# Kernel tuning notes

Measured on AMD Instinct MI355X. Metric: run time of the kernel, lower is better.

## Reference

```python
import jax, jax.numpy as jnp
from jax import lax
import numpy as np

B, C, L = 64, 32, 1549
HID = 256          # LSTM hidden per direction
NH, DK = 8, 64     # n_heads, d_k ; NH*DK = 2*HID = 512
D2 = 2 * HID


def setup_inputs() -> dict:
    key = jax.random.key(0)
    ks = jax.random.split(key, 32)
    r = lambda i, shape: jax.random.normal(ks[i], shape, jnp.float32) * 0.05
    inp = {"x": jax.random.normal(ks[0], (B, C, L), jnp.float32)}
    inp["conv_w"] = r(1, (C, C, 16))
    inp["conv_b"] = r(2, (C,))
    inp["bn_gamma"] = 1.0 + r(3, (C,))
    inp["bn_beta"] = r(4, (C,))
    inp["bn_mean"] = r(5, (C,))
    inp["bn_var"] = jax.random.uniform(ks[6], (C,), jnp.float32, 0.5, 1.5)
    names = [("W_ih0f", (4*HID, C)), ("W_hh0f", (4*HID, HID)), ("b0f", (4*HID,)),
             ("W_ih0b", (4*HID, C)), ("W_hh0b", (4*HID, HID)), ("b0b", (4*HID,)),
             ("W_ih1f", (4*HID, D2)), ("W_hh1f", (4*HID, HID)), ("b1f", (4*HID,)),
             ("W_ih1b", (4*HID, D2)), ("W_hh1b", (4*HID, HID)), ("b1b", (4*HID,)),
             ("Wq", (D2, D2)), ("bq", (D2,)), ("Wk", (D2, D2)), ("bk", (D2,)),
             ("Wv", (D2, D2)), ("bv", (D2,)), ("ln_g", (D2,)), ("ln_b", (D2,)),
             ("fc_w", (1, D2)), ("fc_b", (1,))]
    for j, (n, s) in enumerate(names):
        inp[n] = r(7 + j, s)
    inp["ln_g"] = 1.0 + inp["ln_g"]
    return inp


def _lstm_dir(xg, W_hh, reverse):
    # xg: [B,S,4H] precomputed input-to-gate projections (+biases); PyTorch gate order i,f,g,o
    if reverse:
        xg = xg[:, ::-1]
    Bq = xg.shape[0]
    H = W_hh.shape[1]
    def step(carry, g_t):
        h, c = carry
        g = g_t + h @ W_hh.T
        i, f, gg, o = jnp.split(g, 4, axis=-1)
        c = jax.nn.sigmoid(f) * c + jax.nn.sigmoid(i) * jnp.tanh(gg)
        h = jax.nn.sigmoid(o) * jnp.tanh(c)
        return (h, c), h
    init = (jnp.zeros((Bq, H), xg.dtype), jnp.zeros((Bq, H), xg.dtype))
    _, hs = lax.scan(step, init, jnp.swapaxes(xg, 0, 1))
    hs = jnp.swapaxes(hs, 0, 1)
    return hs[:, ::-1] if reverse else hs


def _bilstm(x, Wif, Whf, bf, Wib, Whb, bb):
    hf = _lstm_dir(jnp.einsum('bsd,gd->bsg', x, Wif) + bf, Whf, False)
    hb = _lstm_dir(jnp.einsum('bsd,gd->bsg', x, Wib) + bb, Whb, True)
    return jnp.concatenate([hf, hb], axis=-1)


def _forward(x, conv_w, conv_b, bn_gamma, bn_beta, bn_mean, bn_var,
             W_ih0f, W_hh0f, b0f, W_ih0b, W_hh0b, b0b,
             W_ih1f, W_hh1f, b1f, W_ih1b, W_hh1b, b1b,
             Wq, bq, Wk, bk, Wv, bv, ln_g, ln_b, fc_w, fc_b):
    # conv1d (k=16, pad=1) + BatchNorm (eval) + relu + maxpool(k=3, stride=3)
    h = lax.conv_general_dilated(x, conv_w, (1,), [(1, 1)],
                                 dimension_numbers=('NCH', 'OIH', 'NCH')) + conv_b[None, :, None]
    h = (h - bn_mean[None, :, None]) * jax.lax.rsqrt(bn_var[None, :, None] + 1e-5) \
        * bn_gamma[None, :, None] + bn_beta[None, :, None]
    h = jax.nn.relu(h)
    h = lax.reduce_window(h, -jnp.inf, lax.max, (1, 1, 3), (1, 1, 3), 'VALID')
    h = jnp.transpose(h, (0, 2, 1))            # [B, S, C]
    # 2-layer bidirectional LSTM (eval: inter-layer dropout inactive)
    out = _bilstm(h, W_ih0f, W_hh0f, b0f, W_ih0b, W_hh0b, b0b)
    out = _bilstm(out, W_ih1f, W_hh1f, b1f, W_ih1b, W_hh1b, b1b)   # [B, S, 512]
    Bq, S, _ = out.shape
    q = (out @ Wq.T + bq).reshape(Bq, S, NH, DK).transpose(0, 2, 1, 3)
    k = (out @ Wk.T + bk).reshape(Bq, S, NH, DK).transpose(0, 2, 1, 3)
    v = (out @ Wv.T + bv).reshape(Bq, S, NH, DK).transpose(0, 2, 1, 3)
    attn = jnp.einsum('bhsd,bhtd->bhst', q, k) / np.sqrt(DK)
    # NOTE: original uses nn.LogSoftmax(dim=1) -> log-softmax over the HEAD axis
    la = jax.nn.log_softmax(attn, axis=1)
    ctx = jnp.einsum('bhst,bhtd->bhsd', la, v)
    ctx = jnp.transpose(ctx, (0, 2, 1, 3)).reshape(Bq, S, D2)
    r = out + ctx
    mu = jnp.mean(r, axis=-1, keepdims=True)
    var = jnp.mean((r - mu) ** 2, axis=-1, keepdims=True)
    r = (r - mu) * jax.lax.rsqrt(var + 1e-5) * ln_g + ln_b
    pooled = jnp.mean(r, axis=1)               # len_reduction='mean'
    return pooled @ fc_w.T + fc_b              # [B, 1]


def reference(x, conv_w, conv_b, bn_gamma, bn_beta, bn_mean, bn_var,
              W_ih0f, W_hh0f, b0f, W_ih0b, W_hh0b, b0b,
              W_ih1f, W_hh1f, b1f, W_ih1b, W_hh1b, b1b,
              Wq, bq, Wk, bk, Wv, bv, ln_g, ln_b, fc_w, fc_b):
    return _forward(x, conv_w, conv_b, bn_gamma, bn_beta, bn_mean, bn_var,
                    W_ih0f, W_hh0f, b0f, W_ih0b, W_hh0b, b0b,
                    W_ih1f, W_hh1f, b1f, W_ih1b, W_hh1b, b1b,
                    Wq, bq, Wk, bk, Wv, bv, ln_g, ln_b, fc_w, fc_b)
```

## Files before the change

### kernel.cpp

```cpp
#include <hip/hip_runtime.h>
#include <hip/hip_bf16.h>
#include <math.h>

#define L_IN 1549
#define S_OUT 512

typedef __hip_bfloat16 bf16;
typedef __attribute__((ext_vector_type(8))) short bfrag;
typedef __attribute__((ext_vector_type(4))) float f32x4;

__device__ __forceinline__ float bfbits2f(unsigned short u) {
    union { unsigned int i; float f; } x;
    x.i = ((unsigned int)u) << 16;
    return x.f;
}
__device__ __forceinline__ unsigned short f2bfbits(float f) {
    union { float f; unsigned int i; } x; x.f = f;
    unsigned int lsb = (x.i >> 16) & 1;
    return (unsigned short)((x.i + 0x7fff + lsb) >> 16);
}
__device__ __forceinline__ float4 cv8(const float* p) {
    float4 u0 = *(const float4*)p;
    float4 u1 = *(const float4*)(p + 4);
    union { float4 f; unsigned short h[8]; } o;
    o.h[0] = f2bfbits(u0.x); o.h[1] = f2bfbits(u0.y);
    o.h[2] = f2bfbits(u0.z); o.h[3] = f2bfbits(u0.w);
    o.h[4] = f2bfbits(u1.x); o.h[5] = f2bfbits(u1.y);
    o.h[6] = f2bfbits(u1.z); o.h[7] = f2bfbits(u1.w);
    return o.f;
}

__device__ __forceinline__ float fast_sig(float x) {
    float e = __builtin_amdgcn_exp2f(-1.442695041f * x);
    return __builtin_amdgcn_rcpf(1.f + e);
}
__device__ __forceinline__ float fast_tanh(float x) {
    float e = __builtin_amdgcn_exp2f(2.885390082f * x);
    return 1.f - 2.f * __builtin_amdgcn_rcpf(1.f + e);
}

#if __has_builtin(__builtin_amdgcn_fdot2_f32_bf16)
typedef __attribute__((ext_vector_type(2))) __bf16 v2bf;
__device__ __forceinline__ float dot2bf(unsigned int w, unsigned int h, float c) {
    union { unsigned int u; v2bf v; } a, b;
    a.u = w; b.u = h;
    return __builtin_amdgcn_fdot2_f32_bf16(a.v, b.v, c, false);
}
#else
__device__ __forceinline__ float dot2bf(unsigned int w, unsigned int h, float c) {
    union { unsigned int i; float f; } w0, w1, h0, h1;
    w0.i = w << 16; w1.i = w & 0xffff0000u;
    h0.i = h << 16; h1.i = h & 0xffff0000u;
    return c + w0.f * h0.f + w1.f * h1.f;
}
#endif

__global__ __launch_bounds__(256) void conv_bn_pool(
    const float* __restrict__ x, const float* __restrict__ w,
    const float* __restrict__ cb, const float* __restrict__ gamma,
    const float* __restrict__ beta, const float* __restrict__ mean,
    const float* __restrict__ var, bf16* __restrict__ h0)
{
    int b  = blockIdx.y;
    int sg = blockIdx.x;
    __shared__ float xs[32][40];
    int tid = threadIdx.x;
    int base = sg * 24;
    for (int i = tid; i < 32 * 40; i += 256) {
        int ci = i / 40, dl = i % 40;
        int l = base - 1 + dl;
        xs[ci][dl] = (l >= 0 && l < L_IN) ? x[(size_t)(b * 32 + ci) * L_IN + l] : 0.f;
    }
    __syncthreads();
    int c = tid & 31, sl = tid >> 5;
    float scale = gamma[c] * rsqrtf(var[c] + 1e-5f);
    float shift = beta[c] - mean[c] * scale;
    float bias = cb[c];
    float acc0 = bias, acc1 = bias, acc2 = bias;
    int off0 = 3 * sl;
    for (int ci = 0; ci < 32; ++ci) {
        const float* wrp = w + (size_t)(c * 32 + ci) * 16;
        float4 w0 = *(const float4*)(wrp);
        float4 w1 = *(const float4*)(wrp + 4);
        float4 w2 = *(const float4*)(wrp + 8);
        float4 w3 = *(const float4*)(wrp + 12);
        float wk[16] = {w0.x, w0.y, w0.z, w0.w, w1.x, w1.y, w1.z, w1.w,
                        w2.x, w2.y, w2.z, w2.w, w3.x, w3.y, w3.z, w3.w};
        const float* xr = &xs[ci][off0];
        #pragma unroll
        for (int kk = 0; kk < 16; ++kk) {
            float xv0 = xr[kk];
            float xv1 = xr[kk + 1];
            float xv2 = xr[kk + 2];
            acc0 += xv0 * wk[kk];
            acc1 += xv1 * wk[kk];
            acc2 += xv2 * wk[kk];
        }
    }
    float y0 = fmaxf(acc0 * scale + shift, 0.f);
    float y1 = fmaxf(acc1 * scale + shift, 0.f);
    float y2 = fmaxf(acc2 * scale + shift, 0.f);
    float best = fmaxf(fmaxf(y0, y1), y2);
    int s = sg * 8 + sl;
    h0[((size_t)b * S_OUT + s) * 32 + c] = __float2bfloat16(best);
}

__global__ void pack_lstm4(
    const float* __restrict__ W0, const float* __restrict__ W1,
    const float* __restrict__ W2, const float* __restrict__ W3,
    unsigned int* __restrict__ outbase)
{
    int set = blockIdx.y;
    const float* W = (set == 0) ? W0 : (set == 1) ? W1 : (set == 2) ? W2 : W3;
    unsigned int* out = outbase + (size_t)set * 131072;
    int i = blockIdx.x * 256 + threadIdx.x;
    int kp, t, col;
    if (i < 102400) {
        kp = i >> 10; col = (i >> 9) & 1; t = i & 511;
    } else if (i < 116736) {
        int j = i - 102400;
        kp = 100 + (j >> 10); t = (j & 1023) >> 1; col = j & 1;
    } else {
        int j = i - 116736;
        kp = 114 + (j >> 10); t = (j & 1023) >> 1; col = j & 1;
    }
    int g = 2 * t + col;
    unsigned int lo = f2bfbits(W[(size_t)g * 256 + 2 * kp]);
    unsigned int hi = f2bfbits(W[(size_t)g * 256 + 2 * kp + 1]);
    out[i] = lo | (hi << 16);
}

__global__ __launch_bounds__(256) void gemm_mfma(
    const bf16* __restrict__ A,
    const float* __restrict__ Bm0, const float* __restrict__ Bm1, const float* __restrict__ Bm2,
    const float* __restrict__ bs0, const float* __restrict__ bs1, const float* __restrict__ bs2,
    bf16* __restrict__ Cm0, bf16* __restrict__ Cm1, bf16* __restrict__ Cm2,
    int M, int N, int K)
{
    int nbn = N >> 7;
    int nbm = M >> 7;
    int lid = blockIdx.x;
    int xcd = lid & 7;
    int slot = lid >> 3;
    int bn = slot % nbn;
    int pair = xcd + 8 * (slot / nbn);
    int bm = pair % nbm;
    int z  = pair / nbm;

    const float* B = (z == 0) ? Bm0 : ((z == 1) ? Bm1 : Bm2);
    const float* bias = (z == 0) ? bs0 : ((z == 1) ? bs1 : bs2);
    bf16* C = (z == 0) ? Cm0 : ((z == 1) ? Cm1 : Cm2);

    __shared__ bf16 As[128 * 32];
    __shared__ bf16 Bs[128 * 32];

    int tid = threadIdx.x;
    int lane = tid & 63;
    int wave = tid >> 6;
    int wm = (wave >> 1) * 64;
    int wn = (wave & 1) * 64;

    int sr = tid >> 2;
    int sc = (tid & 3) * 8;
    const bf16* Ag = A + (size_t)(bm * 128 + sr) * K + sc;
    const float* Bg = B + (size_t)(bn * 128 + sr) * K + sc;

    int fm = lane & 15;
    int fk = (lane >> 4) * 8;

    f32x4 acc[4][4];
    #pragma unroll
    for (int i = 0; i < 4; ++i)
        #pragma unroll
        for (int j = 0; j < 4; ++j) acc[i][j] = (f32x4)(0.f);

    for (int k0 = 0; k0 < K; k0 += 32) {
        float4 a0 = *(const float4*)(Ag + k0);
        float4 a1 = *(const float4*)(Ag + (size_t)64 * K + k0);
        float4 b0 = cv8(Bg + k0);
        float4 b1 = cv8(Bg + (size_t)64 * K + k0);
        __syncthreads();
        *(float4*)(As + sr * 32 + sc)        = a0;
        *(float4*)(As + (sr + 64) * 32 + sc) = a1;
        *(float4*)(Bs + sr * 32 + sc)        = b0;
        *(float4*)(Bs + (sr + 64) * 32 + sc) = b1;
        __syncthreads();

        bfrag af[4], bfr[4];
        #pragma unroll
        for (int i = 0; i < 4; ++i)
            af[i] = *(const bfrag*)(As + (wm + i * 16 + fm) * 32 + fk);
        #pragma unroll
        for (int j = 0; j < 4; ++j)
            bfr[j] = *(const bfrag*)(Bs + (wn + j * 16 + fm) * 32 + fk);
        #pragma unroll
        for (int i = 0; i < 4; ++i)
            #pragma unroll
            for (int j = 0; j < 4; ++j)
                acc[i][j] = __builtin_amdgcn_mfma_f32_16x16x32_bf16(
                    af[i], bfr[j], acc[i][j], 0, 0, 0);
    }

    int rbase = (lane >> 4) * 4;
    #pragma unroll
    for (int j = 0; j < 4; ++j) {
        int n = bn * 128 + wn + j * 16 + (lane & 15);
        float bv = bias[n];
        #pragma unroll
        for (int i = 0; i < 4; ++i) {
            #pragma unroll
            for (int r = 0; r < 4; ++r) {
                int m = bm * 128 + wm + i * 16 + rbase + r;
                C[(size_t)m * N + n] = __float2bfloat16(acc[i][j][r] + bv);
            }
        }
    }
}

__global__ __launch_bounds__(512, 2) void lstm_reg(
    const bf16* __restrict__ xg_f, const bf16* __restrict__ xg_b,
    const unsigned int* __restrict__ Wl, bf16* __restrict__ out)
{
    int u = blockIdx.x;
    int b = u & 63, dir = u >> 6;
    const unsigned int* W = Wl + (size_t)dir * 131072;
    const bf16* xg = dir ? xg_b : xg_f;
    int t = threadIdx.x;

    __shared__ unsigned int lw[14336];
    __shared__ __align__(16) unsigned int hsb[2][128];
    __shared__ float gsh[1024];

    unsigned int wr[200];
    #pragma unroll
    for (int j = 0; j < 200; ++j) wr[j] = W[j * 512 + t];
    for (int i = t; i < 14336; i += 512) lw[i] = W[102400 + i];
    if (t < 128) { hsb[0][t] = 0u; }
    float cst = 0.f;
    __syncthreads();

    const unsigned int* Wst = W + 116736;
    int par = 0;
    unsigned short hb = 0;
    size_t oaddr = 0;
    bool have_out = false;

    for (int step = 0; step < 512; ++step) {
        int ts = dir ? (511 - step) : step;

        uint2 sw[14];
        #pragma unroll
        for (int s = 0; s < 14; ++s)
            sw[s] = *(const uint2*)(Wst + s * 1024 + 2 * t);
        unsigned int xv =
            *(const unsigned int*)(xg + ((size_t)b * 512 + ts) * 1024 + 2 * t);

        const unsigned int* hs = hsb[par];
        float a0 = 0.f, a1 = 0.f;
        #pragma unroll
        for (int q = 0; q < 32; ++q) {
            uint4 hv = *(const uint4*)&hs[q * 4];
            #pragma unroll
            for (int r = 0; r < 4; ++r) {
                int kp = q * 4 + r;
                unsigned int h2 = (&hv.x)[r];
                if (kp < 100) {
                    a0 = dot2bf(wr[kp * 2], h2, a0);
                    a1 = dot2bf(wr[kp * 2 + 1], h2, a1);
                } else if (kp < 114) {
                    uint2 wv = *(const uint2*)&lw[(kp - 100) * 1024 + 2 * t];
                    a0 = dot2bf(wv.x, h2, a0);
                    a1 = dot2bf(wv.y, h2, a1);
                } else {
                    a0 = dot2bf(sw[kp - 114].x, h2, a0);
                    a1 = dot2bf(sw[kp - 114].y, h2, a1);
                }
            }
        }
        a0 += bfbits2f((unsigned short)(xv & 0xffff));
        a1 += bfbits2f((unsigned short)(xv >> 16));

        *(float2*)&gsh[2 * t] = make_float2(a0, a1);
        __syncthreads();

        if (t < 256) {
            float gi = gsh[t], gf = gsh[256 + t], gg = gsh[512 + t], go = gsh[768 + t];
            float si = fast_sig(gi);
            float sf = fast_sig(gf);
            float so = fast_sig(go);
            cst = sf * cst + si * fast_tanh(gg);
            float h = so * fast_tanh(cst);
            hb = f2bfbits(h);
            ((unsigned short*)hsb[par ^ 1])[t] = hb;
            oaddr = ((size_t)b * 512 + ts) * 512 + dir * 256 + t;
            have_out = true;
        }
        __syncthreads();
        if (have_out) {
            *(unsigned short*)(out + oaddr) = hb;
            have_out = false;
        }
        par ^= 1;
    }
}

__global__ __launch_bounds__(256) void vt_transpose(
    const bf16* __restrict__ v, bf16* __restrict__ vt)
{
    __shared__ unsigned short tile[64 * 73];
    int b = blockIdx.z;
    int s0 = blockIdx.x * 64, n0 = blockIdx.y * 64;
    int tid = threadIdx.x;
    #pragma unroll
    for (int u = 0; u < 2; ++u) {
        int idx = tid + u * 256;
        int si = idx >> 3, nj = (idx & 7) << 3;
        bfrag val = *(const bfrag*)(v + ((size_t)(b * 512 + s0 + si)) * 512 + n0 + nj);
        #pragma unroll
        for (int jj = 0; jj < 8; ++jj)
            tile[(nj + jj) * 73 + si] = ((unsigned short*)&val)[jj];
    }
    __syncthreads();
    #pragma unroll
    for (int u = 0; u < 2; ++u) {
        int idx = tid + u * 256;
        int ni = idx >> 3, sj = (idx & 7) << 3;
        unsigned short outv[8];
        #pragma unroll
        for (int jj = 0; jj < 8; ++jj)
            outv[jj] = tile[ni * 73 + sj + jj];
        *(float4*)(vt + (size_t)b * 262144 + (size_t)(n0 + ni) * 512 + s0 + sj) =
            *(float4*)outv;
    }
}

__global__ __launch_bounds__(256, 2) void attention_mfma(
    const bf16* __restrict__ q, const bf16* __restrict__ k,
    const bf16* __restrict__ vt, bf16* r)
{
    int n_ = blockIdx.x;
    int xcd = n_ & 7;
    int slot = n_ >> 3;
    int b = xcd + ((slot >> 4) << 3);
    int s0 = (slot & 15) * 32;
    int tid = threadIdx.x;
    int wave = tid >> 6;
    int sw = wave & 1, dh = wave >> 1;
    int lane = tid & 63;
    int L15 = lane & 15, quad = lane >> 4;

    const bf16* qrow = q + ((size_t)(b * 512 + s0 + sw * 16 + L15)) * 512;
    bfrag qf[8][2];
    #pragma unroll
    for (int h = 0; h < 8; ++h) {
        qf[h][0] = *(const bfrag*)(qrow + h * 64 + quad * 8);
        qf[h][1] = *(const bfrag*)(qrow + h * 64 + 32 + quad * 8);
    }

    f32x4 ctxa[8][2];
    #pragma unroll
    for (int h = 0; h < 8; ++h) {
        ctxa[h][0] = (f32x4)(0.f);
        ctxa[h][1] = (f32x4)(0.f);
    }

    int tperm = ((L15 >> 2) << 3) + (L15 & 3);
    const bf16* kbase = k + (size_t)(b * 512) * 512;
    const bf16* vbase = vt + (size_t)b * 262144;

    for (int tc = 0; tc < 512; tc += 32) {
        f32x4 sa[8][2];
        #pragma unroll
        for (int h = 0; h < 8; ++h) {
            #pragma unroll
            for (int tile = 0; tile < 2; ++tile) {
                const bf16* krow = kbase
                    + (size_t)(tc + tile * 4 + tperm) * 512 + h * 64 + quad * 8;
                bfrag a0 = *(const bfrag*)(krow);
                bfrag a1 = *(const bfrag*)(krow + 32);
                f32x4 acc = __builtin_amdgcn_mfma_f32_16x16x32_bf16(
                    a0, qf[h][0], (f32x4)(0.f), 0, 0, 0);
                acc = __builtin_amdgcn_mfma_f32_16x16x32_bf16(
                    a1, qf[h][1], acc, 0, 0, 0);
                sa[h][tile] = acc;
            }
        }
        bfrag pf[8];
        #pragma unroll
        for (int tile = 0; tile < 2; ++tile) {
            #pragma unroll
            for (int rr = 0; rr < 4; ++rr) {
                float sc[8];
                float m = -1e30f;
                #pragma unroll
                for (int h = 0; h < 8; ++h) {
                    sc[h] = sa[h][tile][rr] * 0.125f;
                    m = fmaxf(m, sc[h]);
                }
                float sum = 0.f;
                #pragma unroll
                for (int h = 0; h < 8; ++h)
                    sum += __builtin_amdgcn_exp2f((sc[h] - m) * 1.442695041f);
                float lse = m + 0.6931471806f * __builtin_amdgcn_logf(sum);
                #pragma unroll
                for (int h = 0; h < 8; ++h)
                    ((unsigned short*)&pf[h])[tile * 4 + rr] = f2bfbits(sc[h] - lse);
            }
        }
        #pragma unroll
        for (int h = 0; h < 8; ++h) {
            #pragma unroll
            for (int dt = 0; dt < 2; ++dt) {
                int n = h * 64 + dh * 32 + dt * 16 + L15;
                bfrag vf = *(const bfrag*)(vbase + (size_t)n * 512 + tc + quad * 8);
                ctxa[h][dt] = __builtin_amdgcn_mfma_f32_16x16x32_bf16(
                    pf[h], vf, ctxa[h][dt], 0, 0, 0);
            }
        }
    }
    #pragma unroll
    for (int h = 0; h < 8; ++h) {
        #pragma unroll
        for (int dt = 0; dt < 2; ++dt) {
            int n = h * 64 + dh * 32 + dt * 16 + L15;
            #pragma unroll
            for (int rr = 0; rr < 4; ++rr) {
                size_t addr =
                    ((size_t)(b * 512 + s0 + sw * 16 + quad * 4 + rr)) * 512 + n;
                float o = __bfloat162float(r[addr]);
                r[addr] = __float2bfloat16(o + ctxa[h][dt][rr]);
            }
        }
    }
}

__global__ __launch_bounds__(512) void ln_pool_fc(
    const bf16* __restrict__ r, const float* __restrict__ g, const float* __restrict__ bt,
    const float* __restrict__ fcw, const float* __restrict__ fcb, float* __restrict__ out)
{
    int b = blockIdx.y;
    int s = blockIdx.x * 8 + (threadIdx.x >> 6);
    int lane = threadIdx.x & 63;
    int n0 = lane * 8;

    float gf[8];
    float btf = 0.f;
    #pragma unroll
    for (int j = 0; j < 8; ++j) {
        float fw = fcw[n0 + j];
        gf[j] = g[n0 + j] * fw;
        btf += bt[n0 + j] * fw;
    }

    bfrag rv = *(const bfrag*)(r + ((size_t)(b * 512 + s)) * 512 + n0);
    float v[8];
    float s1 = 0.f, s2 = 0.f;
    #pragma unroll
    for (int j = 0; j < 8; ++j) {
        v[j] = bfbits2f(((const unsigned short*)&rv)[j]);
        s1 += v[j];
        s2 += v[j] * v[j];
    }
    #pragma unroll
    for (int off = 32; off > 0; off >>= 1) {
        s1 += __shfl_xor(s1, off);
        s2 += __shfl_xor(s2, off);
    }
    float mu = s1 * (1.f / 512.f);
    float var = s2 * (1.f / 512.f) - mu * mu;
    float rs = rsqrtf(var + 1e-5f);

    float d = 0.f;
    #pragma unroll
    for (int j = 0; j < 8; ++j) d += (v[j] - mu) * gf[j];
    #pragma unroll
    for (int off = 32; off > 0; off >>= 1) {
        d += __shfl_down(d, off);
        btf += __shfl_down(btf, off);
    }
    if (lane == 0) {
        float val = d * rs * (1.f / 512.f);
        if (s == 0) val += btf + fcb[0];
        atomicAdd(out + b, val);
    }
}

extern "C" void kernel_launch(void* const* d_in, const int* in_sizes, int n_in,
                              void* d_out, int out_size, void* d_ws, size_t ws_size,
                              hipStream_t stream)
{
    (void)in_sizes; (void)n_in; (void)ws_size;
    const float* x      = (const float*)d_in[0];
    const float* conv_w = (const float*)d_in[1];
    const float* conv_b = (const float*)d_in[2];
    const float* bn_g   = (const float*)d_in[3];
    const float* bn_b   = (const float*)d_in[4];
    const float* bn_m   = (const float*)d_in[5];
    const float* bn_v   = (const float*)d_in[6];
    const float* W_ih0f = (const float*)d_in[7];
    const float* W_hh0f = (const float*)d_in[8];
    const float* b0f    = (const float*)d_in[9];
    const float* W_ih0b = (const float*)d_in[10];
    const float* W_hh0b = (const float*)d_in[11];
    const float* b0b    = (const float*)d_in[12];
    const float* W_ih1f = (const float*)d_in[13];
    const float* W_hh1f = (const float*)d_in[14];
    const float* b1f    = (const float*)d_in[15];
    const float* W_ih1b = (const float*)d_in[16];
    const float* W_hh1b = (const float*)d_in[17];
    const float* b1b    = (const float*)d_in[18];
    const float* Wq = (const float*)d_in[19];
    const float* bq = (const float*)d_in[20];
    const float* Wk = (const float*)d_in[21];
    const float* bk = (const float*)d_in[22];
    const float* Wv = (const float*)d_in[23];
    const float* bv = (const float*)d_in[24];
    const float* ln_g = (const float*)d_in[25];
    const float* ln_b = (const float*)d_in[26];
    const float* fc_w = (const float*)d_in[27];
    const float* fc_b = (const float*)d_in[28];
    float* out = (float*)d_out;

    char* ws = (char*)d_ws;
    bf16* xgf  = (bf16*)ws;
    bf16* xgb  = xgf + 33554432;
    bf16* out0 = (bf16*)(ws + 134217728);
    bf16* out1 = (bf16*)(ws + 167772160);
    bf16* h0   = (bf16*)(ws + 201326592);
    unsigned int* wl0 = (unsigned int*)(ws + 203423744);
    unsigned int* wl1 = wl0 + 262144;
    bf16* qb = xgf;
    bf16* kb = xgf + 16777216;
    bf16* vb = xgb;
    bf16* vtb = out0;

    hipMemsetAsync(d_out, 0, (size_t)out_size * sizeof(float), stream);

    pack_lstm4<<<dim3(512, 4), 256, 0, stream>>>(
        W_hh0f, W_hh0b, W_hh1f, W_hh1b, wl0);

    conv_bn_pool<<<dim3(64, 64), 256, 0, stream>>>(
        x, conv_w, conv_b, bn_g, bn_b, bn_m, bn_v, h0);

    gemm_mfma<<<4096, 256, 0, stream>>>(
        h0, W_ih0f, W_ih0b, nullptr, b0f, b0b, nullptr, xgf, xgb, nullptr,
        32768, 1024, 32);

    lstm_reg<<<128, 512, 0, stream>>>(xgf, xgb, wl0, out0);

    gemm_mfma<<<4096, 256, 0, stream>>>(
        out0, W_ih1f, W_ih1b, nullptr, b1f, b1b, nullptr, xgf, xgb, nullptr,
        32768, 1024, 512);

    lstm_reg<<<128, 512, 0, stream>>>(xgf, xgb, wl1, out1);

    gemm_mfma<<<3072, 256, 0, stream>>>(
        out1, Wq, Wk, Wv, bq, bk, bv, qb, kb, vb,
        32768, 512, 512);

    vt_transpose<<<dim3(8, 8, 64), 256, 0, stream>>>(vb, vtb);

    attention_mfma<<<1024, 256, 0, stream>>>(qb, kb, vtb, out1);

    ln_pool_fc<<<dim3(64, 64), 512, 0, stream>>>(out1, ln_g, ln_b, fc_w, fc_b, out);
}
```

Baseline: 2.775 ms.

## Pre-pack GEMM weights to bf16 once and pad LDS rows

A new kernel converts all seven GEMM weight matrices to bf16 into a workspace buffer once per call. The GEMM kernel then loads B tiles directly as bf16 instead of reading fp32 and converting per tile. This halves B-operand global traffic and drops the repeated conversion work done by every block. Separately, the LDS row stride is padded from 32 to 40 elements to reduce bank conflicts on fragment reads. The cost is one extra small launch plus the extra workspace.

```diff
diff --git a/kernel.cpp b/kernel.cpp
--- a/kernel.cpp
+++ b/kernel.cpp
@@ -18,16 +18,6 @@
     union { float f; unsigned int i; } x; x.f = f;
     unsigned int lsb = (x.i >> 16) & 1;
     return (unsigned short)((x.i + 0x7fff + lsb) >> 16);
-}
-__device__ __forceinline__ float4 cv8(const float* p) {
-    float4 u0 = *(const float4*)p;
-    float4 u1 = *(const float4*)(p + 4);
-    union { float4 f; unsigned short h[8]; } o;
-    o.h[0] = f2bfbits(u0.x); o.h[1] = f2bfbits(u0.y);
-    o.h[2] = f2bfbits(u0.z); o.h[3] = f2bfbits(u0.w);
-    o.h[4] = f2bfbits(u1.x); o.h[5] = f2bfbits(u1.y);
-    o.h[6] = f2bfbits(u1.z); o.h[7] = f2bfbits(u1.w);
-    return o.f;
 }
 
 __device__ __forceinline__ float fast_sig(float x) {
@@ -130,9 +120,29 @@
     out[i] = lo | (hi << 16);
 }
 
+__global__ __launch_bounds__(256) void pack_b7(
+    const float* __restrict__ A0, const float* __restrict__ A1,
+    const float* __restrict__ A2, const float* __restrict__ A3,
+    const float* __restrict__ A4, const float* __restrict__ A5,
+    const float* __restrict__ A6, unsigned short* __restrict__ out)
+{
+    int i = blockIdx.x * 256 + threadIdx.x;
+    const float* src; int j;
+    if      (i <   32768) { src = A0; j = i; }
+    else if (i <   65536) { src = A1; j = i - 32768; }
+    else if (i <  589824) { src = A2; j = i - 65536; }
+    else if (i < 1114112) { src = A3; j = i - 589824; }
+    else if (i < 1376256) { src = A4; j = i - 1114112; }
+    else if (i < 1638400) { src = A5; j = i - 1376256; }
+    else if (i < 1900544) { src = A6; j = i - 1638400; }
+    else return;
+    out[i] = f2bfbits(src[j]);
+}
+
+#define LDA 40
 __global__ __launch_bounds__(256) void gemm_mfma(
     const bf16* __restrict__ A,
-    const float* __restrict__ Bm0, const float* __restrict__ Bm1, const float* __restrict__ Bm2,
+    const bf16* __restrict__ Bm0, const bf16* __restrict__ Bm1, const bf16* __restrict__ Bm2,
     const float* __restrict__ bs0, const float* __restrict__ bs1, const float* __restrict__ bs2,
     bf16* __restrict__ Cm0, bf16* __restrict__ Cm1, bf16* __restrict__ Cm2,
     int M, int N, int K)
@@ -147,12 +157,12 @@
     int bm = pair % nbm;
     int z  = pair / nbm;
 
-    const float* B = (z == 0) ? Bm0 : ((z == 1) ? Bm1 : Bm2);
+    const bf16* B = (z == 0) ? Bm0 : ((z == 1) ? Bm1 : Bm2);
     const float* bias = (z == 0) ? bs0 : ((z == 1) ? bs1 : bs2);
     bf16* C = (z == 0) ? Cm0 : ((z == 1) ? Cm1 : Cm2);
 
-    __shared__ bf16 As[128 * 32];
-    __shared__ bf16 Bs[128 * 32];
+    __shared__ bf16 As[128 * LDA];
+    __shared__ bf16 Bs[128 * LDA];
 
     int tid = threadIdx.x;
     int lane = tid & 63;
@@ -163,7 +173,7 @@
     int sr = tid >> 2;
     int sc = (tid & 3) * 8;
     const bf16* Ag = A + (size_t)(bm * 128 + sr) * K + sc;
-    const float* Bg = B + (size_t)(bn * 128 + sr) * K + sc;
+    const bf16* Bg = B + (size_t)(bn * 128 + sr) * K + sc;
 
     int fm = lane & 15;
     int fk = (lane >> 4) * 8;
@@ -177,22 +187,22 @@
     for (int k0 = 0; k0 < K; k0 += 32) {
         float4 a0 = *(const float4*)(Ag + k0);
         float4 a1 = *(const float4*)(Ag + (size_t)64 * K + k0);
-        float4 b0 = cv8(Bg + k0);
-        float4 b1 = cv8(Bg + (size_t)64 * K + k0);
+        float4 b0 = *(const float4*)(Bg + k0);
+        float4 b1 = *(const float4*)(Bg + (size_t)64 * K + k0);
         __syncthreads();
-        *(float4*)(As + sr * 32 + sc)        = a0;
-        *(float4*)(As + (sr + 64) * 32 + sc) = a1;
-        *(float4*)(Bs + sr * 32 + sc)        = b0;
-        *(float4*)(Bs + (sr + 64) * 32 + sc) = b1;
+        *(float4*)(As + sr * LDA + sc)        = a0;
+        *(float4*)(As + (sr + 64) * LDA + sc) = a1;
+        *(float4*)(Bs + sr * LDA + sc)        = b0;
+        *(float4*)(Bs + (sr + 64) * LDA + sc) = b1;
         __syncthreads();
 
         bfrag af[4], bfr[4];
         #pragma unroll
         for (int i = 0; i < 4; ++i)
-            af[i] = *(const bfrag*)(As + (wm + i * 16 + fm) * 32 + fk);
+            af[i] = *(const bfrag*)(As + (wm + i * 16 + fm) * LDA + fk);
         #pragma unroll
         for (int j = 0; j < 4; ++j)
-            bfr[j] = *(const bfrag*)(Bs + (wn + j * 16 + fm) * 32 + fk);
+            bfr[j] = *(const bfrag*)(Bs + (wn + j * 16 + fm) * LDA + fk);
         #pragma unroll
         for (int i = 0; i < 4; ++i)
             #pragma unroll
@@ -529,6 +539,7 @@
     bf16* h0   = (bf16*)(ws + 201326592);
     unsigned int* wl0 = (unsigned int*)(ws + 203423744);
     unsigned int* wl1 = wl0 + 262144;
+    bf16* wpk  = (bf16*)(ws + 205520896);
     bf16* qb = xgf;
     bf16* kb = xgf + 16777216;
     bf16* vb = xgb;
@@ -539,24 +550,27 @@
     pack_lstm4<<<dim3(512, 4), 256, 0, stream>>>(
         W_hh0f, W_hh0b, W_hh1f, W_hh1b, wl0);
 
+    pack_b7<<<7424, 256, 0, stream>>>(
+        W_ih0f, W_ih0b, W_ih1f, W_ih1b, Wq, Wk, Wv, (unsigned short*)wpk);
+
     conv_bn_pool<<<dim3(64, 64), 256, 0, stream>>>(
         x, conv_w, conv_b, bn_g, bn_b, bn_m, bn_v, h0);
 
     gemm_mfma<<<4096, 256, 0, stream>>>(
-        h0, W_ih0f, W_ih0b, nullptr, b0f, b0b, nullptr, xgf, xgb, nullptr,
+        h0, wpk, wpk + 32768, nullptr, b0f, b0b, nullptr, xgf, xgb, nullptr,
         32768, 1024, 32);
 
     lstm_reg<<<128, 512, 0, stream>>>(xgf, xgb, wl0, out0);
 
     gemm_mfma<<<4096, 256, 0, stream>>>(
-        out0, W_ih1f, W_ih1b, nullptr, b1f, b1b, nullptr, xgf, xgb, nullptr,
-        32768, 1024, 512);
+        out0, wpk + 65536, wpk + 589824, nullptr, b1f, b1b, nullptr,
+        xgf, xgb, nullptr, 32768, 1024, 512);
 
     lstm_reg<<<128, 512, 0, stream>>>(xgf, xgb, wl1, out1);
 
     gemm_mfma<<<3072, 256, 0, stream>>>(
-        out1, Wq, Wk, Wv, bq, bk, bv, qb, kb, vb,
-        32768, 512, 512);
+        out1, wpk + 1114112, wpk + 1376256, wpk + 1638400, bq, bk, bv,
+        qb, kb, vb, 32768, 512, 512);
 
     vt_transpose<<<dim3(8, 8, 64), 256, 0, stream>>>(vb, vtb);
 
```

Result: no change. 2.734 ms (-1.5%).
